# Kernel tuning notes

Measured on AMD Instinct MI355X. Metric: run time of the kernel, lower is better.

The kernel has to match this reference:

```python
import jax, jax.numpy as jnp
import numpy as np

EPS = 1e-12  # F.normalize eps


def _norm_adj(flow):
    # flow: (T, C, C). PyG gcn_norm with self-loops on the dense cosine-sim graph.
    T = flow.shape[0]
    x = flow.reshape(T, -1)                                  # (T, N)
    xn = x / jnp.clip(jnp.linalg.norm(x, axis=1, keepdims=True), EPS)
    A = xn.T @ xn                                            # (N, N) cosine sims
    N = A.shape[0]
    deg = A.sum(axis=0) + 1.0                                # +1 from added self-loop weight
    dinv = jnp.where(deg > 0, jax.lax.rsqrt(deg), 0.0)
    return (A + jnp.eye(N, dtype=A.dtype)) * dinv[:, None] * dinv[None, :]


def setup_inputs() -> dict:
    key = jax.random.key(0)
    ks = jax.random.split(key, 8)
    B, T, C, E = 8, 24, 64, 32
    H = 32
    O = 32
    return {
        "Flow": jax.random.normal(ks[0], (B, T, C, C), dtype=jnp.float32),
        "Edge": jax.random.normal(ks[1], (B, C, C, E), dtype=jnp.float32),
        "W0": jax.random.normal(ks[2], (E, H), dtype=jnp.float32) * 0.1,
        "b0": jax.random.normal(ks[3], (H,), dtype=jnp.float32) * 0.1,
        "W1": jax.random.normal(ks[4], (H, H), dtype=jnp.float32) * 0.1,
        "b1": jax.random.normal(ks[5], (H,), dtype=jnp.float32) * 0.1,
        "W2": jax.random.normal(ks[6], (H, O), dtype=jnp.float32) * 0.1,
        "b2": jax.random.normal(ks[7], (O,), dtype=jnp.float32) * 0.1,
    }


def reference(Flow, Edge, W0, b0, W1, b1, W2, b2):
    B, C, _, E = Edge.shape

    def per_batch(flow, edge):
        A = _norm_adj(flow)                                  # (N, N)
        x = edge.reshape(C * C, E)                           # (N, E)
        for W, b in ((W0, b0), (W1, b1), (W2, b2)):
            x = jax.nn.relu(A @ (x @ W) + b)
        return x.reshape(C, C, -1)

    return jax.vmap(per_batch)(Flow, Edge)                   # (B, C, C, out)
```

## Files before the change

### kernel.cpp

```cpp
#include <hip/hip_runtime.h>

#define BB 8
#define TT 24
#define NN 4096
#define HH 32
#define JT 64
#define UPB (TT*HH)
#define CTRS 16

__global__ __launch_bounds__(256) void k_phase1(const float* __restrict__ Flow,
                                                const float* __restrict__ Edge,
                                                const float* __restrict__ W0,
                                                float* __restrict__ rn,
                                                float* __restrict__ s,
                                                float* __restrict__ uz ,
                                                float* __restrict__ z0raw) {
    const int blk = blockIdx.x;
    const int tid = threadIdx.x;

    if (blk < BB * TT) {
        const float4* x = (const float4*)(Flow + (size_t)blk * NN);
        float sq = 0.f, sm = 0.f;
#pragma unroll
        for (int i = 0; i < 4; ++i) {
            float4 v = x[tid + i * 256];
            sq += v.x * v.x + v.y * v.y + v.z * v.z + v.w * v.w;
            sm += v.x + v.y + v.z + v.w;
        }
#pragma unroll
        for (int off = 32; off > 0; off >>= 1) {
            sq += __shfl_down(sq, off);
            sm += __shfl_down(sm, off);
        }
        __shared__ float rss[4], rsm[4];
        int wave = tid >> 6, lane = tid & 63;
        if (lane == 0) { rss[wave] = sq; rsm[wave] = sm; }
        __syncthreads();
        if (tid == 0) {
            float tss = rss[0] + rss[1] + rss[2] + rss[3];
            float tsm = rsm[0] + rsm[1] + rsm[2] + rsm[3];
            float r = 1.0f / fmaxf(sqrtf(tss), 1e-12f);
            rn[blk] = r;
            s[blk] = tsm * r;
        }
        int gid = blk * 256 + tid;
        if (gid < 3 * BB * TT * HH + 3 * BB * CTRS) uz[gid] = 0.f;
    } else {
        const int g = blk - BB * TT;
        const int b = g >> 6;
        const int j0 = (g & 63) * JT;

        __shared__ float xs[JT][33];
        __shared__ float Ws[32][32];
        for (int i = tid; i < 1024; i += 256) Ws[i >> 5][i & 31] = W0[i];
        {
            const float4* eb = (const float4*)(Edge + ((size_t)b * NN + j0) * HH);
#pragma unroll
            for (int k = 0; k < 2; ++k) {
                int i = tid + k * 256;
                float4 v = eb[i];
                int r0 = i >> 3, c0 = (i & 7) * 4;
                xs[r0][c0] = v.x; xs[r0][c0 + 1] = v.y; xs[r0][c0 + 2] = v.z; xs[r0][c0 + 3] = v.w;
            }
        }
        __syncthreads();
        const int r = tid >> 2;
        const int h0 = (tid & 3) * 8;
        float zr[8];
#pragma unroll
        for (int hh = 0; hh < 8; ++hh) {
            float acc = 0.f;
#pragma unroll
            for (int e = 0; e < 32; ++e) acc += xs[r][e] * Ws[e][h0 + hh];
            zr[hh] = acc;
        }
        float* zb = z0raw + ((size_t)b * NN + j0 + r) * HH + h0;
        ((float4*)zb)[0] = make_float4(zr[0], zr[1], zr[2], zr[3]);
        ((float4*)zb)[1] = make_float4(zr[4], zr[5], zr[6], zr[7]);
    }
}

__global__ __launch_bounds__(256) void k_mega(const float* __restrict__ Flow,
                                              const float* __restrict__ z0raw,
                                              const float* __restrict__ rn,
                                              const float* __restrict__ s,
                                              const float* __restrict__ W1,
                                              const float* __restrict__ W2,
                                              const float* __restrict__ b0,
                                              const float* __restrict__ b1,
                                              const float* __restrict__ b2,
                                              float* __restrict__ u,
                                              unsigned* __restrict__ ctr,
                                              float* __restrict__ out) {
    const int blk = blockIdx.x;
    const int b = blk >> 6;
    const int j0 = (blk & 63) * JT;
    const int tid = threadIdx.x;

    __shared__ float xns[TT][JT];
    __shared__ float zs[JT][33];
    __shared__ float xs[JT][33];
    __shared__ float W1s[32][32];
    __shared__ float W2s[32][32];
    __shared__ float us[TT][32];
    __shared__ float sS[TT];
    __shared__ float b0s[32], b1s[32], b2s[32];

    if (tid < TT) sS[tid] = s[b * TT + tid];
    if (tid < 32) { b0s[tid] = b0[tid]; b1s[tid] = b1[tid]; b2s[tid] = b2[tid]; }
    for (int i = tid; i < 1024; i += 256) { W1s[i >> 5][i & 31] = W1[i]; W2s[i >> 5][i & 31] = W2[i]; }
    {
        const float4* zt = (const float4*)(z0raw + ((size_t)b * NN + j0) * HH);
#pragma unroll
        for (int k = 0; k < 2; ++k) {
            int i = tid + k * 256;
            float4 v = zt[i];
            int r0 = i >> 3, c0 = (i & 7) * 4;
            zs[r0][c0] = v.x; zs[r0][c0 + 1] = v.y; zs[r0][c0 + 2] = v.z; zs[r0][c0 + 3] = v.w;
        }
    }
    {
        const float* flb = Flow + (size_t)b * TT * NN + j0;
        for (int i = tid; i < TT * (JT / 4); i += 256) {
            int t = i >> 4, c0 = (i & 15) * 4;
            float4 v = ((const float4*)(flb + t * NN))[i & 15];
            float rt = rn[b * TT + t];
            xns[t][c0] = v.x * rt; xns[t][c0 + 1] = v.y * rt;
            xns[t][c0 + 2] = v.z * rt; xns[t][c0 + 3] = v.w * rt;
        }
    }
    __syncthreads();

    const int r = tid >> 2;
    const int h0 = (tid & 3) * 8;
    float deg = 1.0f;
#pragma unroll
    for (int t = 0; t < TT; ++t) deg += xns[t][r] * sS[t];
    const float di = (deg > 0.f) ? rsqrtf(deg) : 0.f;
#pragma unroll
    for (int hh = 0; hh < 8; ++hh) zs[r][h0 + hh] *= di;
    __syncthreads();

    float* u0 = u + b * UPB;
    float* u1 = u0 + BB * UPB;
    float* u2 = u1 + BB * UPB;

#define U_PART(dst)                                                        \
    {                                                                      \
        _Pragma("unroll")                                                  \
        for (int k = 0; k < 3; ++k) {                                      \
            int p = tid + k * 256;                                         \
            int t = p >> 5, h = p & 31;                                    \
            float acc = 0.f;                                               \
            _Pragma("unroll 8")                                            \
            for (int rr = 0; rr < JT; ++rr) acc += xns[t][rr] * zs[rr][h]; \
            atomicAdd(&(dst)[t * HH + h], acc);                            \
        }                                                                  \
    }

#define BAR(phase)                                                                  \
    {                                                                               \
        __syncthreads();                \
        if (tid == 0) {                                                             \
            unsigned* c = ctr + ((phase) * BB + b) * CTRS;                          \
            __hip_atomic_fetch_add(c, 1u, __ATOMIC_RELAXED, __HIP_MEMORY_SCOPE_AGENT); \
            while (__hip_atomic_load(c, __ATOMIC_RELAXED, __HIP_MEMORY_SCOPE_AGENT) < 64u) \
                __builtin_amdgcn_s_sleep(4);                                        \
        }                                                                           \
        __syncthreads();                                                            \
    }

#define LOAD_US(src)                                                                \
    {                                                                               \
        _Pragma("unroll")                                                           \
        for (int k = 0; k < 3; ++k) {                                               \
            int p = tid + k * 256;                                                  \
            us[p >> 5][p & 31] = __hip_atomic_load(&(src)[p], __ATOMIC_RELAXED,     \
                                                   __HIP_MEMORY_SCOPE_AGENT);       \
        }                                                                           \
        __syncthreads();                                                            \
    }

    U_PART(u0);
    BAR(0);
    LOAD_US(u0);

#pragma unroll
    for (int hh = 0; hh < 8; ++hh) {
        int h = h0 + hh;
        float acc = 0.f;
#pragma unroll
        for (int t = 0; t < TT; ++t) acc += xns[t][r] * us[t][h];
        xs[r][h] = fmaxf(di * (acc + zs[r][h]) + b0s[h], 0.f);
    }
#pragma unroll
    for (int hh = 0; hh < 8; ++hh) {
        float acc = 0.f;
#pragma unroll
        for (int e = 0; e < 32; ++e) acc += xs[r][e] * W1s[e][h0 + hh];
        zs[r][h0 + hh] = di * acc;
    }
    __syncthreads();
    U_PART(u1);
    BAR(1);
    LOAD_US(u1);

#pragma unroll
    for (int hh = 0; hh < 8; ++hh) {
        int h = h0 + hh;
        float acc = 0.f;
#pragma unroll
        for (int t = 0; t < TT; ++t) acc += xns[t][r] * us[t][h];
        xs[r][h] = fmaxf(di * (acc + zs[r][h]) + b1s[h], 0.f);
    }
#pragma unroll
    for (int hh = 0; hh < 8; ++hh) {
        float acc = 0.f;
#pragma unroll
        for (int e = 0; e < 32; ++e) acc += xs[r][e] * W2s[e][h0 + hh];
        zs[r][h0 + hh] = di * acc;
    }
    __syncthreads();
    U_PART(u2);
    BAR(2);
    LOAD_US(u2);

    float o[8];
#pragma unroll
    for (int hh = 0; hh < 8; ++hh) {
        int h = h0 + hh;
        float acc = 0.f;
#pragma unroll
        for (int t = 0; t < TT; ++t) acc += xns[t][r] * us[t][h];
        o[hh] = fmaxf(di * (acc + zs[r][h]) + b2s[h], 0.f);
    }
    float* orow = out + ((size_t)b * NN + j0 + r) * HH + h0;
    ((float4*)orow)[0] = make_float4(o[0], o[1], o[2], o[3]);
    ((float4*)orow)[1] = make_float4(o[4], o[5], o[6], o[7]);

#undef U_PART
#undef BAR
#undef LOAD_US
}

extern "C" void kernel_launch(void* const* d_in, const int* in_sizes, int n_in,
                              void* d_out, int out_size, void* d_ws, size_t ws_size,
                              hipStream_t stream) {
    const float* Flow = (const float*)d_in[0];
    const float* Edge = (const float*)d_in[1];
    const float* W0 = (const float*)d_in[2];
    const float* b0 = (const float*)d_in[3];
    const float* W1 = (const float*)d_in[4];
    const float* b1 = (const float*)d_in[5];
    const float* W2 = (const float*)d_in[6];
    const float* b2 = (const float*)d_in[7];
    float* out = (float*)d_out;

    float* ws = (float*)d_ws;
    float* rn    = ws;
    float* s     = rn + BB * TT;
    float* z0raw = s + BB * TT;
    float* u     = z0raw + (size_t)BB * NN * HH;
    unsigned* ctr = (unsigned*)(u + 3 * BB * UPB);

    k_phase1<<<dim3(BB * TT + 512), 256, 0, stream>>>(Flow, Edge, W0, rn, s, u, z0raw);
    k_mega<<<dim3(512), 256, 0, stream>>>(Flow, z0raw, rn, s, W1, W2, b0, b1, b2,
                                          u, ctr, out);
}
```

Measured before the change: 46.55 us.

## Fuse first-layer Edge@W0 into mega kernel and halve node tile size

The x@W0 projection moves out of the first kernel and into the persistent mega kernel, which now loads Edge and W0 directly. This removes the z0raw intermediate buffer and its global write and read round trip. The node tile shrinks from 64 to 32 rows, giving 1024 blocks with a 4-blocks-per-CU launch bound. Each thread now handles 4 output features instead of 8. The trade-off is twice as many atomicAdds into the u buffers and 128 participants per batch at each spin barrier, which depends on all 1024 blocks being resident at once.

Result: slower. 110.5 us (+137.5%).

```diff
diff --git a/kernel.cpp b/kernel.cpp
--- a/kernel.cpp
+++ b/kernel.cpp
@@ -4,141 +4,108 @@
 #define TT 24
 #define NN 4096
 #define HH 32
-#define JT 64
+#define JT 32
+#define NBLK (NN/JT)
 #define UPB (TT*HH)
 #define CTRS 16
 
-__global__ __launch_bounds__(256) void k_phase1(const float* __restrict__ Flow,
-                                                const float* __restrict__ Edge,
-                                                const float* __restrict__ W0,
-                                                float* __restrict__ rn,
-                                                float* __restrict__ s,
-                                                float* __restrict__ uz ,
-                                                float* __restrict__ z0raw) {
+__global__ __launch_bounds__(256) void k_norm(const float* __restrict__ Flow,
+                                              float* __restrict__ rn,
+                                              float* __restrict__ s,
+                                              float* __restrict__ uz) {
     const int blk = blockIdx.x;
     const int tid = threadIdx.x;
-
-    if (blk < BB * TT) {
-        const float4* x = (const float4*)(Flow + (size_t)blk * NN);
-        float sq = 0.f, sm = 0.f;
-#pragma unroll
-        for (int i = 0; i < 4; ++i) {
-            float4 v = x[tid + i * 256];
-            sq += v.x * v.x + v.y * v.y + v.z * v.z + v.w * v.w;
-            sm += v.x + v.y + v.z + v.w;
-        }
-#pragma unroll
-        for (int off = 32; off > 0; off >>= 1) {
-            sq += __shfl_down(sq, off);
-            sm += __shfl_down(sm, off);
-        }
-        __shared__ float rss[4], rsm[4];
-        int wave = tid >> 6, lane = tid & 63;
-        if (lane == 0) { rss[wave] = sq; rsm[wave] = sm; }
-        __syncthreads();
-        if (tid == 0) {
-            float tss = rss[0] + rss[1] + rss[2] + rss[3];
-            float tsm = rsm[0] + rsm[1] + rsm[2] + rsm[3];
-            float r = 1.0f / fmaxf(sqrtf(tss), 1e-12f);
-            rn[blk] = r;
-            s[blk] = tsm * r;
-        }
-        int gid = blk * 256 + tid;
-        if (gid < 3 * BB * TT * HH + 3 * BB * CTRS) uz[gid] = 0.f;
-    } else {
-        const int g = blk - BB * TT;
-        const int b = g >> 6;
-        const int j0 = (g & 63) * JT;
-
-        __shared__ float xs[JT][33];
-        __shared__ float Ws[32][32];
-        for (int i = tid; i < 1024; i += 256) Ws[i >> 5][i & 31] = W0[i];
-        {
-            const float4* eb = (const float4*)(Edge + ((size_t)b * NN + j0) * HH);
-#pragma unroll
-            for (int k = 0; k < 2; ++k) {
-                int i = tid + k * 256;
-                float4 v = eb[i];
-                int r0 = i >> 3, c0 = (i & 7) * 4;
-                xs[r0][c0] = v.x; xs[r0][c0 + 1] = v.y; xs[r0][c0 + 2] = v.z; xs[r0][c0 + 3] = v.w;
-            }
-        }
-        __syncthreads();
-        const int r = tid >> 2;
-        const int h0 = (tid & 3) * 8;
-        float zr[8];
-#pragma unroll
-        for (int hh = 0; hh < 8; ++hh) {
-            float acc = 0.f;
-#pragma unroll
-            for (int e = 0; e < 32; ++e) acc += xs[r][e] * Ws[e][h0 + hh];
-            zr[hh] = acc;
-        }
-        float* zb = z0raw + ((size_t)b * NN + j0 + r) * HH + h0;
-        ((float4*)zb)[0] = make_float4(zr[0], zr[1], zr[2], zr[3]);
-        ((float4*)zb)[1] = make_float4(zr[4], zr[5], zr[6], zr[7]);
-    }
+    const float4* x = (const float4*)(Flow + (size_t)blk * NN);
+    float sq = 0.f, sm = 0.f;
+#pragma unroll
+    for (int i = 0; i < 4; ++i) {
+        float4 v = x[tid + i * 256];
+        sq += v.x * v.x + v.y * v.y + v.z * v.z + v.w * v.w;
+        sm += v.x + v.y + v.z + v.w;
+    }
+#pragma unroll
+    for (int off = 32; off > 0; off >>= 1) {
+        sq += __shfl_down(sq, off);
+        sm += __shfl_down(sm, off);
+    }
+    __shared__ float rss[4], rsm[4];
+    int wave = tid >> 6, lane = tid & 63;
+    if (lane == 0) { rss[wave] = sq; rsm[wave] = sm; }
+    __syncthreads();
+    if (tid == 0) {
+        float tss = rss[0] + rss[1] + rss[2] + rss[3];
+        float tsm = rsm[0] + rsm[1] + rsm[2] + rsm[3];
+        float r = 1.0f / fmaxf(sqrtf(tss), 1e-12f);
+        rn[blk] = r;
+        s[blk] = tsm * r;
+    }
+    int gid = blk * 256 + tid;
+    if (gid < 3 * BB * TT * HH + 3 * BB * CTRS) uz[gid] = 0.f;
 }
 
-__global__ __launch_bounds__(256) void k_mega(const float* __restrict__ Flow,
-                                              const float* __restrict__ z0raw,
-                                              const float* __restrict__ rn,
-                                              const float* __restrict__ s,
-                                              const float* __restrict__ W1,
-                                              const float* __restrict__ W2,
-                                              const float* __restrict__ b0,
-                                              const float* __restrict__ b1,
-                                              const float* __restrict__ b2,
-                                              float* __restrict__ u,
-                                              unsigned* __restrict__ ctr,
-                                              float* __restrict__ out) {
+__global__ __launch_bounds__(256, 4) void k_mega(const float* __restrict__ Flow,
+                                                 const float* __restrict__ Edge,
+                                                 const float* __restrict__ W0,
+                                                 const float* __restrict__ W1,
+                                                 const float* __restrict__ W2,
+                                                 const float* __restrict__ b0,
+                                                 const float* __restrict__ b1,
+                                                 const float* __restrict__ b2,
+                                                 const float* __restrict__ rn,
+                                                 const float* __restrict__ s,
+                                                 float* __restrict__ u,
+                                                 unsigned* __restrict__ ctr,
+                                                 float* __restrict__ out) {
     const int blk = blockIdx.x;
-    const int b = blk >> 6;
-    const int j0 = (blk & 63) * JT;
+    const int b = blk >> 7;
+    const int j0 = (blk & (NBLK - 1)) * JT;
     const int tid = threadIdx.x;
 
     __shared__ float xns[TT][JT];
-    __shared__ float zs[JT][33];
-    __shared__ float xs[JT][33];
-    __shared__ float W1s[32][32];
-    __shared__ float W2s[32][32];
-    __shared__ float us[TT][32];
-    __shared__ float sS[TT];
+    __shared__ float zs[JT][HH + 1];
+    __shared__ float xs[JT][HH + 1];
+    __shared__ float W0s[32][32], W1s[32][32], W2s[32][32];
+    __shared__ float us[TT][HH];
+    __shared__ float sS[TT], rnS[TT];
     __shared__ float b0s[32], b1s[32], b2s[32];
 
-    if (tid < TT) sS[tid] = s[b * TT + tid];
+    if (tid < TT) { sS[tid] = s[b * TT + tid]; rnS[tid] = rn[b * TT + tid]; }
     if (tid < 32) { b0s[tid] = b0[tid]; b1s[tid] = b1[tid]; b2s[tid] = b2[tid]; }
-    for (int i = tid; i < 1024; i += 256) { W1s[i >> 5][i & 31] = W1[i]; W2s[i >> 5][i & 31] = W2[i]; }
+    __syncthreads();
+
+    for (int i = tid; i < 1024; i += 256) {
+        W0s[i >> 5][i & 31] = W0[i];
+        W1s[i >> 5][i & 31] = W1[i];
+        W2s[i >> 5][i & 31] = W2[i];
+    }
     {
-        const float4* zt = (const float4*)(z0raw + ((size_t)b * NN + j0) * HH);
-#pragma unroll
-        for (int k = 0; k < 2; ++k) {
-            int i = tid + k * 256;
-            float4 v = zt[i];
-            int r0 = i >> 3, c0 = (i & 7) * 4;
-            zs[r0][c0] = v.x; zs[r0][c0 + 1] = v.y; zs[r0][c0 + 2] = v.z; zs[r0][c0 + 3] = v.w;
-        }
-    }
-    {
-        const float* flb = Flow + (size_t)b * TT * NN + j0;
-        for (int i = tid; i < TT * (JT / 4); i += 256) {
-            int t = i >> 4, c0 = (i & 15) * 4;
-            float4 v = ((const float4*)(flb + t * NN))[i & 15];
-            float rt = rn[b * TT + t];
-            xns[t][c0] = v.x * rt; xns[t][c0 + 1] = v.y * rt;
-            xns[t][c0 + 2] = v.z * rt; xns[t][c0 + 3] = v.w * rt;
-        }
-    }
-    __syncthreads();
-
-    const int r = tid >> 2;
-    const int h0 = (tid & 3) * 8;
+        float4 v = ((const float4*)(Edge + ((size_t)b * NN + j0) * HH))[tid];
+        int r0 = tid >> 3, c0 = (tid & 7) * 4;
+        xs[r0][c0] = v.x; xs[r0][c0 + 1] = v.y; xs[r0][c0 + 2] = v.z; xs[r0][c0 + 3] = v.w;
+    }
+    if (tid < TT * (JT / 4)) {
+        int t = tid >> 3, c0 = (tid & 7) * 4;
+        float4 v = ((const float4*)(Flow + (size_t)b * TT * NN + (size_t)t * NN + j0))[tid & 7];
+        float rt = rnS[t];
+        xns[t][c0] = v.x * rt; xns[t][c0 + 1] = v.y * rt;
+        xns[t][c0 + 2] = v.z * rt; xns[t][c0 + 3] = v.w * rt;
+    }
+    __syncthreads();
+
+    const int r = tid >> 3;
+    const int h0 = (tid & 7) * 4;
     float deg = 1.0f;
 #pragma unroll
     for (int t = 0; t < TT; ++t) deg += xns[t][r] * sS[t];
     const float di = (deg > 0.f) ? rsqrtf(deg) : 0.f;
-#pragma unroll
-    for (int hh = 0; hh < 8; ++hh) zs[r][h0 + hh] *= di;
+
+#pragma unroll
+    for (int hh = 0; hh < 4; ++hh) {
+        float acc = 0.f;
+#pragma unroll
+        for (int e = 0; e < 32; ++e) acc += xs[r][e] * W0s[e][h0 + hh];
+        zs[r][h0 + hh] = di * acc;
+    }
     __syncthreads();
 
     float* u0 = u + b * UPB;
@@ -164,7 +131,7 @@
         if (tid == 0) {                                                             \
             unsigned* c = ctr + ((phase) * BB + b) * CTRS;                          \
             __hip_atomic_fetch_add(c, 1u, __ATOMIC_RELAXED, __HIP_MEMORY_SCOPE_AGENT); \
-            while (__hip_atomic_load(c, __ATOMIC_RELAXED, __HIP_MEMORY_SCOPE_AGENT) < 64u) \
+            while (__hip_atomic_load(c, __ATOMIC_RELAXED, __HIP_MEMORY_SCOPE_AGENT) < (unsigned)NBLK) \
                 __builtin_amdgcn_s_sleep(4);                                        \
         }                                                                           \
         __syncthreads();                                                            \
@@ -186,7 +153,7 @@
     LOAD_US(u0);
 
 #pragma unroll
-    for (int hh = 0; hh < 8; ++hh) {
+    for (int hh = 0; hh < 4; ++hh) {
         int h = h0 + hh;
         float acc = 0.f;
 #pragma unroll
@@ -194,7 +161,7 @@
         xs[r][h] = fmaxf(di * (acc + zs[r][h]) + b0s[h], 0.f);
     }
 #pragma unroll
-    for (int hh = 0; hh < 8; ++hh) {
+    for (int hh = 0; hh < 4; ++hh) {
         float acc = 0.f;
 #pragma unroll
         for (int e = 0; e < 32; ++e) acc += xs[r][e] * W1s[e][h0 + hh];
@@ -206,7 +173,7 @@
     LOAD_US(u1);
 
 #pragma unroll
-    for (int hh = 0; hh < 8; ++hh) {
+    for (int hh = 0; hh < 4; ++hh) {
         int h = h0 + hh;
         float acc = 0.f;
 #pragma unroll
@@ -214,7 +181,7 @@
         xs[r][h] = fmaxf(di * (acc + zs[r][h]) + b1s[h], 0.f);
     }
 #pragma unroll
-    for (int hh = 0; hh < 8; ++hh) {
+    for (int hh = 0; hh < 4; ++hh) {
         float acc = 0.f;
 #pragma unroll
         for (int e = 0; e < 32; ++e) acc += xs[r][e] * W2s[e][h0 + hh];
@@ -225,9 +192,9 @@
     BAR(2);
     LOAD_US(u2);
 
-    float o[8];
-#pragma unroll
-    for (int hh = 0; hh < 8; ++hh) {
+    float o[4];
+#pragma unroll
+    for (int hh = 0; hh < 4; ++hh) {
         int h = h0 + hh;
         float acc = 0.f;
 #pragma unroll
@@ -236,7 +203,6 @@
     }
     float* orow = out + ((size_t)b * NN + j0 + r) * HH + h0;
     ((float4*)orow)[0] = make_float4(o[0], o[1], o[2], o[3]);
-    ((float4*)orow)[1] = make_float4(o[4], o[5], o[6], o[7]);
 
 #undef U_PART
 #undef BAR
@@ -257,13 +223,12 @@
     float* out = (float*)d_out;
 
     float* ws = (float*)d_ws;
-    float* rn    = ws;
-    float* s     = rn + BB * TT;
-    float* z0raw = s + BB * TT;
-    float* u     = z0raw + (size_t)BB * NN * HH;
+    float* rn = ws;
+    float* s  = rn + BB * TT;
+    float* u  = s + BB * TT;
     unsigned* ctr = (unsigned*)(u + 3 * BB * UPB);
 
-    k_phase1<<<dim3(BB * TT + 512), 256, 0, stream>>>(Flow, Edge, W0, rn, s, u, z0raw);
-    k_mega<<<dim3(512), 256, 0, stream>>>(Flow, z0raw, rn, s, W1, W2, b0, b1, b2,
-                                          u, ctr, out);
+    k_norm<<<dim3(BB * TT), 256, 0, stream>>>(Flow, rn, s, u);
+    k_mega<<<dim3(BB * NBLK), 256, 0, stream>>>(Flow, Edge, W0, W1, W2,
+                                                b0, b1, b2, rn, s, u, ctr, out);
 }
```
